# Kernel tuning notes

Measured on AMD Instinct MI355X. Metric: run time of the kernel, lower is better.

## Reference

```python
import jax, jax.numpy as jnp
import numpy as np

EPS = 1e-12  # VERY_SMALL_NUMBER
LN_EPS = 1e-5
N, NFEAT, NHID, A, P, HOPS = 50000, 256, 128, 32, 4, 2


def setup_inputs() -> dict:
    key = jax.random.key(0)
    ks = jax.random.split(key, 16)
    def w(i, shape, scale=0.05):
        return jax.random.normal(ks[i], shape, dtype=jnp.float32) * scale
    return {
        "x": jax.random.normal(ks[0], (N, NFEAT), dtype=jnp.float32),
        # input_mapper: Linear(nfeat,nhid) -> ReLU -> Linear(nhid,nhid)
        "im_w1": w(1, (NFEAT, NHID)), "im_b1": jnp.zeros((NHID,), jnp.float32),
        "im_w2": w(2, (NHID, NHID)),  "im_b2": jnp.zeros((NHID,), jnp.float32),
        # AnchorGraphLearner
        "anchors": w(3, (A, NHID), 1.0),
        "ml_w1": w(4, (P, 2 * NHID, NHID)), "ml_b1": jnp.zeros((P, NHID), jnp.float32),
        "ml_w2": w(5, (P, NHID)),            "ml_b2": jnp.zeros((P,), jnp.float32),
        # AnchorGNNLayer weights (xavier in torch; scaled randn here)
        "enc_w": w(6, (HOPS, NHID, NHID)), "enc_b": jnp.zeros((HOPS, NHID), jnp.float32),
        # LayerNorm
        "ln_g": jnp.ones((NHID,), jnp.float32), "ln_b": jnp.zeros((NHID,), jnp.float32),
        # classifier: Linear -> PReLU(nhid) -> Linear(nhid,2)
        "cls_w1": w(7, (NHID, NHID)), "cls_b1": jnp.zeros((NHID,), jnp.float32),
        "prelu_a": jnp.full((NHID,), 0.25, jnp.float32),
        "cls_w2": w(8, (NHID, 2)),   "cls_b2": jnp.zeros((2,), jnp.float32),
    }


def _forward(x, im_w1, im_b1, im_w2, im_b2, anchors, ml_w1, ml_b1, ml_w2, ml_b2,
             enc_w, enc_b, ln_g, ln_b, cls_w1, cls_b1, prelu_a, cls_w2, cls_b2):
    nhid = im_w2.shape[-1]
    # input_mapper (dropout is identity in eval)
    h = jnp.maximum(x @ im_w1 + im_b1, 0.0) @ im_w2 + im_b2  # [N, nhid]
    x_loc = h

    # --- AnchorGraphLearner: fused form of cat([x_i, a_j]) @ W1 ---
    Wx, Wa = ml_w1[:, :nhid, :], ml_w1[:, nhid:, :]  # each [P, nhid, nhid]
    attn = jnp.zeros((h.shape[0], anchors.shape[0]), h.dtype)
    for p in range(ml_w1.shape[0]):  # small fixed head count
        hx = h @ Wx[p]                               # [N, nhid]
        ha = anchors @ Wa[p]                         # [A, nhid]
        hid = jnp.maximum(hx[:, None, :] + ha[None, :, :] + ml_b1[p], 0.0)  # [N, A, nhid]
        attn = attn + jax.nn.sigmoid(hid @ ml_w2[p] + ml_b2[p])            # [N, A]
    adj = attn / ml_w1.shape[0]  # mean over heads, [N, A]

    # --- AnchorGNNLayer stack (anchor_mp normalized double matmul) ---
    node_norm = adj / jnp.maximum(adj.sum(axis=0, keepdims=True), EPS)     # col-normalized [N, A]
    anchor_norm = adj / jnp.maximum(adj.sum(axis=1, keepdims=True), EPS)   # row-normalized [N, A]
    xc = h
    for i in range(enc_w.shape[0]):
        support = xc @ enc_w[i]                          # [N, nhid]
        agg = node_norm.T @ support                      # [A, nhid]
        xc = jnp.maximum(anchor_norm @ agg + enc_b[i], 0.0)

    # residual + LayerNorm
    z = xc + x_loc
    mu = z.mean(axis=-1, keepdims=True)
    var = ((z - mu) ** 2).mean(axis=-1, keepdims=True)
    z = (z - mu) * jax.lax.rsqrt(var + LN_EPS) * ln_g + ln_b

    def classifier(t):
        t1 = t @ cls_w1 + cls_b1
        t1 = jnp.where(t1 > 0, t1, prelu_a * t1)  # PReLU(nhid)
        return t1 @ cls_w2 + cls_b2

    pred = classifier(z)                 # [N, 2]
    anchor_logits = classifier(anchors)  # [A, 2]
    anchor_vec = anchors[None]           # [1, A, nhid] (matches unsqueeze(0))
    return (pred, z, anchor_vec, anchor_logits)


def reference(x, im_w1, im_b1, im_w2, im_b2, anchors, ml_w1, ml_b1, ml_w2, ml_b2,
              enc_w, enc_b, ln_g, ln_b, cls_w1, cls_b1, prelu_a, cls_w2, cls_b2):
    return _forward(x, im_w1, im_b1, im_w2, im_b2, anchors, ml_w1, ml_b1, ml_w2, ml_b2,
                    enc_w, enc_b, ln_g, ln_b, cls_w1, cls_b1, prelu_a, cls_w2, cls_b2)
```

## Files before the change

kernel.cpp:

```cpp
#include <hip/hip_runtime.h>
#include <math.h>

#define NN 50000
#define FEAT 256
#define HID 128
#define NA 32
#define NP 4
#define TM 64
#define NBLK 782
#define LDA 132
#define EPSS 1e-12f
#define LN_EPS 1e-5f

typedef unsigned short u16;
typedef __attribute__((ext_vector_type(8))) short bf16x8;
typedef __attribute__((ext_vector_type(4))) float f32x4;

#define ADJ_F   0
#define RS_F    1600000
#define CS_F    1650000
#define AGG0_F  1650032
#define AGG1_F  1654128
#define HB_F    1658256
#define FLAG_F  1674640
#define F_END   1674672
#define XC_U   (2 * F_END)
#define SUP_U  (XC_U + NN * HID)
#define PW_U   (SUP_U + NN * HID)
#define PW_TOT 165638
#define WS_NEED_BYTES ((size_t)(PW_U + PW_TOT) * 2ULL)

#define PK_IMW1T  0
#define PK_IMW2T  32768
#define PK_MLW1T  49152
#define PK_ENCWT  114688
#define PK_CLSW1T 147456
#define PK_IMB1   163840
#define PK_IMB2   163968
#define PK_MLW2   164096
#define PK_ENCB   164608
#define PK_LNG    164864
#define PK_LNB    164992
#define PK_CLSB1  165120
#define PK_PRELU  165248
#define PK_CLSW2  165376
#define PK_CLSB2  165632
#define PK_MLB2   165634
#define PK_TOTAL  165638

#define PRED_OFF 0
#define Z_OFF    100000
#define AV_OFF   6500000
#define AL_OFF   6504096
#define OUT_TOT  6504160

__device__ __constant__ int kNel[19] = {
    NN * FEAT, FEAT * HID, HID, HID * HID, HID, NA * HID,
    NP * 2 * HID * HID, NP * HID, NP * HID, NP, 2 * HID * HID, 2 * HID,
    HID, HID, HID * HID, HID, HID, HID * 2, 2};

#define TSEG_TOT 163840
__device__ __constant__ int tLen[9]  = {32768,16384,16384,16384,16384,16384,16384,16384,16384};
__device__ __constant__ int tDst[9]  = {PK_IMW1T,PK_IMW2T,PK_MLW1T,PK_MLW1T+16384,
                                        PK_MLW1T+32768,PK_MLW1T+49152,PK_ENCWT,
                                        PK_ENCWT+16384,PK_CLSW1T};
__device__ __constant__ int tSrcT[9] = {1,3,6,6,6,6,10,10,14};
__device__ __constant__ int tBase[9] = {0,0,0,32768,65536,98304,0,16384,0};
#define VSEG_TOT 1798
__device__ __constant__ int vLen[11] = {128,128,512,256,128,128,128,128,256,2,4};
__device__ __constant__ int vDst[11] = {PK_IMB1,PK_IMB2,PK_MLW2,PK_ENCB,PK_LNG,PK_LNB,
                                        PK_CLSB1,PK_PRELU,PK_CLSW2,PK_CLSB2,PK_MLB2};
__device__ __constant__ int vSrcT[11]= {2,4,8,11,12,13,15,16,17,18,9};

struct P19 { const void* q[19]; };

__device__ __forceinline__ float b2f(u16 u) {
    union { float f; unsigned int i; } v; v.i = ((unsigned int)u) << 16; return v.f;
}
__device__ __forceinline__ u16 f2b(float f) {
    union { float f; unsigned int i; } v; v.f = f;
    unsigned int x = v.i;
    x += 0x7fffu + ((x >> 16) & 1u);
    return (u16)(x >> 16);
}
__device__ __forceinline__ float ldf(const void* p, size_t i, int fl) {
    if (fl == 1) return ((const float*)p)[i];
    if (fl == 0) return b2f(((const u16*)p)[i]);
    return 0.f;
}

__global__ __launch_bounds__(256) void k_detect_all(P19 a, int* __restrict__ flags) {
    __shared__ int sHi[256], sE[256], sO[256];
    const int b = blockIdx.x;
    const u16* p = (const u16*)a.q[b];
    const int M = (kNel[b] < 8192) ? kNel[b] : 8192;
    int cHi = 0, cE = 0, cO = 0;
    for (int j = threadIdx.x; j < M; j += 256) {
        const u16 v = p[j];
        if (j & 1) cO += (v != 0);
        else { cE += (v != 0); cHi += (((v >> 7) & 0xFF) >= 200); }
    }
    sHi[threadIdx.x] = cHi; sE[threadIdx.x] = cE; sO[threadIdx.x] = cO;
    __syncthreads();
    for (int s = 128; s > 0; s >>= 1) {
        if (threadIdx.x < (unsigned)s) {
            sHi[threadIdx.x] += sHi[threadIdx.x + s];
            sE[threadIdx.x]  += sE[threadIdx.x + s];
            sO[threadIdx.x]  += sO[threadIdx.x + s];
        }
        __syncthreads();
    }
    if (threadIdx.x == 0) {
        int f;
        if (sE[0] == 0 && sO[0] == 0) f = 2;
        else if (sHi[0] >= 4 || sE[0] == 0) f = 1;
        else f = 0;
        flags[b] = f;
    }
}

__global__ __launch_bounds__(256) void k_convT(P19 a, const int* __restrict__ flags,
                                               u16* __restrict__ pw) {
    int idx = blockIdx.x * 256 + threadIdx.x;
    if (idx >= TSEG_TOT) return;
    int off = idx, s = 0;
    while (off >= tLen[s]) { off -= tLen[s]; ++s; }
    int n, k;
    if (s == 0) { n = off >> 8; k = off & 255; }
    else        { n = off >> 7; k = off & 127; }
    const int si = tSrcT[s];
    pw[tDst[s] + off] = f2b(ldf(a.q[si], (size_t)tBase[s] + (size_t)k * 128 + n,
                                flags[si]));
}

__global__ __launch_bounds__(256) void k_convV(P19 a, const int* __restrict__ flags,
                                               u16* __restrict__ pw) {
    for (int idx = threadIdx.x; idx < VSEG_TOT; idx += 256) {
        int off = idx, s = 0;
        while (off >= vLen[s]) { off -= vLen[s]; ++s; }
        const int si = vSrcT[s];
        pw[vDst[s] + off] = f2b(ldf(a.q[si], off, flags[si]));
    }
}

__device__ __forceinline__ void mfma_64x128(const u16* As, const u16* Bt,
                                            f32x4 acc[8], int lane, int rowBase) {
    const int lr = lane & 15, lq = lane >> 4;
#pragma unroll
    for (int kc = 0; kc < 4; ++kc) {
        bf16x8 a = *(const bf16x8*)(As + (rowBase + lr) * 136 + kc * 32 + lq * 8);
#pragma unroll
        for (int t = 0; t < 8; ++t) {
            bf16x8 b = *(const bf16x8*)(Bt + (t * 16 + lr) * 136 + kc * 32 + lq * 8);
            acc[t] = __builtin_amdgcn_mfma_f32_16x16x32_bf16(a, b, acc[t], 0, 0, 0);
        }
    }
}

__global__ __launch_bounds__(256) void k_gemm2(const void* __restrict__ A,
                                               const u16* __restrict__ pw,
                                               float* __restrict__ outh,
                                               const int* __restrict__ flags) {
    __shared__ __align__(16) u16 As[64 * 136];
    __shared__ __align__(16) u16 Bt[128 * 136];
    const int fA = flags[0];
    const int tid = threadIdx.x;
    const int row0 = blockIdx.x * TM;
    const int lane = tid & 63, wv = tid >> 6, rowBase = wv * 16;
    const int lr = lane & 15, lq = lane >> 4;
    f32x4 acc[8];
    const f32x4 z4 = {0.f, 0.f, 0.f, 0.f};
#pragma unroll
    for (int t = 0; t < 8; ++t) acc[t] = z4;

    for (int kc = 0; kc < 2; ++kc) {
        for (int i = tid; i < 64 * 32; i += 256) {
            const int m = i >> 5, k4 = (i & 31) << 2;
            const int g = row0 + m;
            ushort4 o; o.x = 0; o.y = 0; o.z = 0; o.w = 0;
            if (g < NN) {
                const size_t idx = (size_t)g * FEAT + kc * 128 + k4;
                if (fA == 1) {
                    float4 v = *(const float4*)((const float*)A + idx);
                    o.x = f2b(v.x); o.y = f2b(v.y); o.z = f2b(v.z); o.w = f2b(v.w);
                } else {
                    o = *(const ushort4*)((const u16*)A + idx);
                }
            }
            *(ushort4*)&As[m * 136 + k4] = o;
        }
        for (int i = tid; i < 128 * 32; i += 256) {
            const int n = i >> 5, k4 = (i & 31) << 2;
            *(ushort4*)&Bt[n * 136 + k4] =
                *(const ushort4*)(pw + PK_IMW1T + (size_t)n * FEAT + kc * 128 + k4);
        }
        __syncthreads();
        mfma_64x128(As, Bt, acc, lane, rowBase);
        __syncthreads();
    }
#pragma unroll
    for (int t = 0; t < 8; ++t) {
        const int col = t * 16 + lr;
        const float bv = b2f(pw[PK_IMB1 + col]);
#pragma unroll
        for (int r = 0; r < 4; ++r)
            As[(rowBase + lq * 4 + r) * 136 + col] = f2b(fmaxf(acc[t][r] + bv, 0.f));
    }
    for (int i = tid; i < 128 * 32; i += 256) {
        const int n = i >> 5, k4 = (i & 31) << 2;
        *(ushort4*)&Bt[n * 136 + k4] =
            *(const ushort4*)(pw + PK_IMW2T + (size_t)n * HID + k4);
    }
    __syncthreads();
    f32x4 acc2[8];
#pragma unroll
    for (int t = 0; t < 8; ++t) acc2[t] = z4;
    mfma_64x128(As, Bt, acc2, lane, rowBase);
#pragma unroll
    for (int t = 0; t < 8; ++t) {
        const int col = t * 16 + lr;
        const float bv = b2f(pw[PK_IMB2 + col]);
#pragma unroll
        for (int r = 0; r < 4; ++r) {
            const int g = row0 + rowBase + lq * 4 + r;
            if (g < NN) outh[(size_t)g * HID + col] = acc2[t][r] + bv;
        }
    }
}

__global__ __launch_bounds__(128) void k_pre(const void* __restrict__ anchors,
                                             const void* __restrict__ ml_w1,
                                             const void* __restrict__ ml_b1,
                                             float* __restrict__ hb,
                                             const int* __restrict__ flags) {
    __shared__ float sa[HID];
    const int fAn = flags[5], fW1 = flags[6], fB1 = flags[7];
    const int p = blockIdx.x >> 5, a = blockIdx.x & 31, k = threadIdx.x;
    sa[k] = ldf(anchors, a * HID + k, fAn);
    __syncthreads();
    float acc = ldf(ml_b1, p * HID + k, fB1);
    const size_t wbase = ((size_t)p * 2 * HID + HID) * HID + k;
#pragma unroll 4
    for (int j = 0; j < HID; ++j)
        acc += sa[j] * ldf(ml_w1, wbase + (size_t)j * HID, fW1);
    hb[p * (NA * HID) + k * NA + a] = acc;
}

__global__ __launch_bounds__(128) void k_wc(const float* __restrict__ hb,
                                            const u16* __restrict__ pw,
                                            float* __restrict__ wc) {
    __shared__ float red[128];
    const int p = blockIdx.x, tid = threadIdx.x;
    const int a = tid & 31, q = tid >> 5;
    float s = 0.f;
    for (int k = q * 32; k < q * 32 + 32; ++k)
        s += b2f(pw[PK_MLW2 + p * HID + k]) * hb[(size_t)p * (NA * HID) + k * NA + a];
    red[tid] = 0.5f * s;
    __syncthreads();
    if (tid < 32)
        wc[p * NA + tid] = red[tid] + red[tid + 32] + red[tid + 64] + red[tid + 96];
}

__global__ __launch_bounds__(256) void k_anchor(const void* __restrict__ anchors,
                                                const void* __restrict__ cls_w1,
                                                const void* __restrict__ cls_b1,
                                                const void* __restrict__ prelu_a,
                                                const void* __restrict__ cls_w2,
                                                const void* __restrict__ cls_b2,
                                                float* __restrict__ out,
                                                const int* __restrict__ flags) {
    __shared__ float sa[2][HID];
    __shared__ float st1[2][HID];
    const int fAn = flags[5], fW1 = flags[14], fB1 = flags[15];
    const int fPa = flags[16], fW2 = flags[17], fB2 = flags[18];
    const int tid = threadIdx.x;
    const int a0 = blockIdx.x * 2;
    const int half = tid >> 7, k = tid & 127;
    sa[half][k] = ldf(anchors, (a0 + half) * HID + k, fAn);
    __syncthreads();
    float acc = ldf(cls_b1, k, fB1);
#pragma unroll 4
    for (int j = 0; j < HID; ++j) acc += sa[half][j] * ldf(cls_w1, j * HID + k, fW1);
    const float pa = ldf(prelu_a, k, fPa);
    st1[half][k] = acc > 0.f ? acc : pa * acc;
    __syncthreads();
    if (tid < 4) {
        const int aa = tid >> 1, c = tid & 1;
        float s = ldf(cls_b2, c, fB2);
        for (int j = 0; j < HID; ++j) s += st1[aa][j] * ldf(cls_w2, j * 2 + c, fW2);
        out[AL_OFF + (a0 + aa) * 2 + c] = s;
    }
    if (blockIdx.x == 0) {
        for (int i = tid; i < NA * HID; i += 256)
            out[AV_OFF + i] = ldf(anchors, i, fAn);
    }
}

__global__ __launch_bounds__(256) void k_fattn(const float* __restrict__ h,
                                               const u16* __restrict__ pw,
                                               const float* __restrict__ hb,
                                               const float* __restrict__ wc,
                                               float* __restrict__ adj,
                                               float* __restrict__ rowsum,
                                               float* __restrict__ csPart,
                                               float* __restrict__ part) {
    __shared__ __align__(16) u16 Bt[128 * 136];
    __shared__ float hws[HID];
    __shared__ float wcs[NA];
    __shared__ float swr[4][NA];
    float* hbf = (float*)&Bt[64 * 136];
    const int tid = threadIdx.x;
    const int row0 = blockIdx.x * TM;
    const int lane = tid & 63, wv = tid >> 6, rowBase = wv * 16;
    const int lr = lane & 15, lq = lane >> 4;
    const int g = tid & 3, myrow = tid >> 2;
    const int a0 = g * 8;

    bf16x8 afr[4];
    {
        const int gr = row0 + rowBase + lr;
#pragma unroll
        for (int kc = 0; kc < 4; ++kc) {
            bf16x8 t;
            if (gr < NN) {
                const float* src = h + (size_t)gr * HID + kc * 32 + lq * 8;
                float4 v0 = *(const float4*)src;
                float4 v1 = *(const float4*)(src + 4);
                t[0] = (short)f2b(v0.x); t[1] = (short)f2b(v0.y);
                t[2] = (short)f2b(v0.z); t[3] = (short)f2b(v0.w);
                t[4] = (short)f2b(v1.x); t[5] = (short)f2b(v1.y);
                t[6] = (short)f2b(v1.z); t[7] = (short)f2b(v1.w);
            } else {
#pragma unroll
                for (int j = 0; j < 8; ++j) t[j] = 0;
            }
            afr[kc] = t;
        }
    }

    float adjacc[8];
#pragma unroll
    for (int j = 0; j < 8; ++j) adjacc[j] = 0.f;

    for (int p = 0; p < NP; ++p) {
        __syncthreads();
        for (int i = tid; i < 128 * 32; i += 256) {
            const int n = i >> 5, k4 = (i & 31) << 2;
            *(ushort4*)&Bt[n * 136 + k4] =
                *(const ushort4*)(pw + PK_MLW1T + p * 16384 + n * 128 + k4);
        }
        if (tid < HID) hws[tid] = 0.5f * b2f(pw[PK_MLW2 + p * HID + tid]);
        if (tid < NA) wcs[tid] = wc[p * NA + tid];
        __syncthreads();

        f32x4 acc[8];
        const f32x4 z4 = {0.f, 0.f, 0.f, 0.f};
#pragma unroll
        for (int t = 0; t < 8; ++t) acc[t] = z4;
#pragma unroll
        for (int kc = 0; kc < 4; ++kc)
#pragma unroll
            for (int t = 0; t < 8; ++t) {
                bf16x8 b = *(const bf16x8*)(Bt + (t * 16 + lr) * 136 + kc * 32 + lq * 8);
                acc[t] = __builtin_amdgcn_mfma_f32_16x16x32_bf16(afr[kc], b, acc[t], 0, 0, 0);
            }
        __syncthreads();
#pragma unroll
        for (int t = 0; t < 8; ++t)
#pragma unroll
            for (int r = 0; r < 4; ++r)
                Bt[(rowBase + lq * 4 + r) * 136 + t * 16 + lr] = f2b(acc[t][r]);
        {
            const float4* hbp4 = (const float4*)(hb + (size_t)p * (NA * HID));
#pragma unroll
            for (int j = 0; j < 4; ++j)
                ((float4*)hbf)[tid + j * 256] = hbp4[tid + j * 256];
        }
        __syncthreads();

        const float b2v = b2f(pw[PK_MLB2 + p]);
        float sabs[8], wh = 0.f;
#pragma unroll
        for (int j = 0; j < 8; ++j) sabs[j] = 0.f;

#pragma unroll 4
        for (int kp = 0; kp < 64; ++kp) {
            const unsigned hx2 = *(const unsigned*)&Bt[myrow * 136 + kp * 2];
            union { unsigned u; float f; } u0, u1;
            u0.u = hx2 << 16;
            u1.u = hx2 & 0xffff0000u;
            const float f0 = u0.f, f1 = u1.f;
            const float2 hw2 = *(const float2*)&hws[kp * 2];
            wh = fmaf(hw2.x, f0, wh);
            wh = fmaf(hw2.y, f1, wh);
            const float4 c00 = *(const float4*)&hbf[(kp * 2) * NA + a0];
            const float4 c01 = *(const float4*)&hbf[(kp * 2) * NA + a0 + 4];
            const float4 c10 = *(const float4*)&hbf[(kp * 2 + 1) * NA + a0];
            const float4 c11 = *(const float4*)&hbf[(kp * 2 + 1) * NA + a0 + 4];
            sabs[0] = fmaf(hw2.x, fabsf(f0 + c00.x), sabs[0]);
            sabs[1] = fmaf(hw2.x, fabsf(f0 + c00.y), sabs[1]);
            sabs[2] = fmaf(hw2.x, fabsf(f0 + c00.z), sabs[2]);
            sabs[3] = fmaf(hw2.x, fabsf(f0 + c00.w), sabs[3]);
            sabs[4] = fmaf(hw2.x, fabsf(f0 + c01.x), sabs[4]);
            sabs[5] = fmaf(hw2.x, fabsf(f0 + c01.y), sabs[5]);
            sabs[6] = fmaf(hw2.x, fabsf(f0 + c01.z), sabs[6]);
            sabs[7] = fmaf(hw2.x, fabsf(f0 + c01.w), sabs[7]);
            sabs[0] = fmaf(hw2.y, fabsf(f1 + c10.x), sabs[0]);
            sabs[1] = fmaf(hw2.y, fabsf(f1 + c10.y), sabs[1]);
            sabs[2] = fmaf(hw2.y, fabsf(f1 + c10.z), sabs[2]);
            sabs[3] = fmaf(hw2.y, fabsf(f1 + c10.w), sabs[3]);
            sabs[4] = fmaf(hw2.y, fabsf(f1 + c11.x), sabs[4]);
            sabs[5] = fmaf(hw2.y, fabsf(f1 + c11.y), sabs[5]);
            sabs[6] = fmaf(hw2.y, fabsf(f1 + c11.z), sabs[6]);
            sabs[7] = fmaf(hw2.y, fabsf(f1 + c11.w), sabs[7]);
        }
#pragma unroll
        for (int j = 0; j < 8; ++j) {
            const float s = wh + wcs[a0 + j] + b2v + sabs[j];
            adjacc[j] += 0.25f / (1.f + __expf(-s));
        }
    }

    const int grow = row0 + myrow;
    if (grow >= NN) {
#pragma unroll
        for (int j = 0; j < 8; ++j) adjacc[j] = 0.f;
    }
    if (grow < NN) {
        float* dst = adj + (size_t)grow * NA + a0;
        *(float4*)dst = make_float4(adjacc[0], adjacc[1], adjacc[2], adjacc[3]);
        *(float4*)(dst + 4) = make_float4(adjacc[4], adjacc[5], adjacc[6], adjacc[7]);
    }
    float rs = 0.f;
#pragma unroll
    for (int j = 0; j < 8; ++j) rs += adjacc[j];
    rs += __shfl_xor(rs, 1);
    rs += __shfl_xor(rs, 2);
    if (g == 0 && grow < NN) rowsum[grow] = rs;
    __syncthreads();
#pragma unroll
    for (int kc = 0; kc < 4; ++kc)
        *(bf16x8*)&Bt[(rowBase + lr) * 136 + kc * 32 + lq * 8] = afr[kc];
    float* adjTe = (float*)&Bt[64 * 136];
#pragma unroll
    for (int j = 0; j < 8; ++j)
        adjTe[myrow * 33 + a0 + j] = adjacc[j];
#pragma unroll
    for (int st = 4; st <= 32; st <<= 1)
#pragma unroll
        for (int j = 0; j < 8; ++j) adjacc[j] += __shfl_xor(adjacc[j], st);
    if (lane < 4) {
#pragma unroll
        for (int j = 0; j < 8; ++j) swr[wv][lane * 8 + j] = adjacc[j];
    }
    __syncthreads();
    if (tid < NA)
        csPart[tid * NBLK + blockIdx.x] =
            swr[0][tid] + swr[1][tid] + swr[2][tid] + swr[3][tid];
    const int aA = (tid & 15) * 2, kA = (tid >> 4) * 8;
    float acc2[2][8];
#pragma unroll
    for (int ia = 0; ia < 2; ++ia)
#pragma unroll
        for (int j = 0; j < 8; ++j) acc2[ia][j] = 0.f;
#pragma unroll 4
    for (int n = 0; n < TM; ++n) {
        const float a0v = adjTe[n * 33 + aA], a1v = adjTe[n * 33 + aA + 1];
        ushort4 u0 = *(const ushort4*)&Bt[n * 136 + kA];
        ushort4 u1 = *(const ushort4*)&Bt[n * 136 + kA + 4];
        float sv[8] = {b2f(u0.x), b2f(u0.y), b2f(u0.z), b2f(u0.w),
                       b2f(u1.x), b2f(u1.y), b2f(u1.z), b2f(u1.w)};
#pragma unroll
        for (int j = 0; j < 8; ++j) {
            acc2[0][j] += a0v * sv[j];
            acc2[1][j] += a1v * sv[j];
        }
    }
    float* pdst = part + (size_t)blockIdx.x * (NA * HID);
#pragma unroll
    for (int ia = 0; ia < 2; ++ia) {
        *(float4*)&pdst[(aA + ia) * HID + kA] =
            make_float4(acc2[ia][0], acc2[ia][1], acc2[ia][2], acc2[ia][3]);
        *(float4*)&pdst[(aA + ia) * HID + kA + 4] =
            make_float4(acc2[ia][4], acc2[ia][5], acc2[ia][6], acc2[ia][7]);
    }
}

__global__ __launch_bounds__(256) void k_cs_red(const float* __restrict__ csPart,
                                                float* __restrict__ colsum) {
    __shared__ float red[256];
    const int a = blockIdx.x, tid = threadIdx.x;
    float s = 0.f;
    for (int b = tid; b < NBLK; b += 256) s += csPart[a * NBLK + b];
    red[tid] = s;
    __syncthreads();
    for (int st = 128; st > 0; st >>= 1) {
        if (tid < st) red[tid] += red[tid + st];
        __syncthreads();
    }
    if (tid == 0) colsum[a] = red[0];
}

__global__ __launch_bounds__(256) void k_Tred(const float* __restrict__ part,
                                              float* __restrict__ T) {
    __shared__ float red[256];
    const int jj = threadIdx.x & 15, bq = threadIdx.x >> 4;
    const int j = blockIdx.x * 16 + jj;
    float s = 0.f;
#pragma unroll 8
    for (int b = bq; b < NBLK; b += 16) s += part[(size_t)b * (NA * HID) + j];
    red[threadIdx.x] = s;
    __syncthreads();
    if (bq == 0) {
        float t = 0.f;
#pragma unroll
        for (int q = 0; q < 16; ++q) t += red[q * 16 + jj];
        T[j] = t;
    }
}

__global__ __launch_bounds__(128) void k_small(const float* __restrict__ T,
                                               const u16* __restrict__ pw,
                                               const int hop,
                                               float* __restrict__ agg) {
    __shared__ float tr[HID];
    const int a = blockIdx.x, n = threadIdx.x;
    tr[n] = T[a * HID + n];
    __syncthreads();
    const u16* w = pw + PK_ENCWT + hop * HID * HID + n * HID;
    float s = 0.f;
#pragma unroll 4
    for (int j4 = 0; j4 < HID; j4 += 4) {
        ushort4 u = *(const ushort4*)(w + j4);
        s += tr[j4] * b2f(u.x) + tr[j4 + 1] * b2f(u.y) +
             tr[j4 + 2] * b2f(u.z) + tr[j4 + 3] * b2f(u.w);
    }
    agg[a * HID + n] = s;
}

__global__ __launch_bounds__(256) void k_e2a(const float* __restrict__ adj,
                                             const float* __restrict__ rowsum,
                                             const float* __restrict__ colsum,
                                             const float* __restrict__ agg,
                                             const u16* __restrict__ pw,
                                             float* __restrict__ part) {
    __shared__ float aggn[NA][LDA];
    __shared__ float adjT[TM][NA + 1];
    __shared__ __align__(8) u16 xcs[TM * 136];
    __shared__ float csl[NA], rsl[TM];
    const int tid = threadIdx.x;
    const int row0 = blockIdx.x * TM;
    const int n0 = (tid & 31) * 4, m0 = (tid >> 5) * 8;
    const int a0 = (tid & 15) * 2, k0 = (tid >> 4) * 8;

    if (tid < NA) csl[tid] = fmaxf(colsum[tid], EPSS);
    if (tid >= 64 && tid < 128) {
        const int m = tid - 64, g = row0 + m;
        rsl[m] = (g < NN) ? 1.f / fmaxf(rowsum[g], EPSS) : 0.f;
    }
    for (int i = tid; i < TM * NA; i += 256) {
        const int m = i >> 5, a = i & 31, g = row0 + m;
        adjT[m][a] = (g < NN) ? adj[(size_t)g * NA + a] : 0.f;
    }
    __syncthreads();
    for (int i = tid; i < (NA * HID) / 4; i += 256) {
        const int a = i >> 5, k4 = (i & 31) << 2;
        float4 v = *(const float4*)(agg + a * HID + k4);
        const float inv = 1.f / csl[a];
        v.x *= inv; v.y *= inv; v.z *= inv; v.w *= inv;
        *(float4*)&aggn[a][k4] = v;
    }
    float bv[4];
#pragma unroll
    for (int j = 0; j < 4; ++j) bv[j] = b2f(pw[PK_ENCB + n0 + j]);
    __syncthreads();
    float acc[8][4];
#pragma unroll
    for (int i = 0; i < 8; ++i)
#pragma unroll
        for (int j = 0; j < 4; ++j) acc[i][j] = 0.f;
    for (int a = 0; a < NA; ++a) {
        float4 gv = *(const float4*)&aggn[a][n0];
        float gvv[4] = {gv.x, gv.y, gv.z, gv.w};
#pragma unroll
        for (int i = 0; i < 8; ++i) {
            const float av = adjT[m0 + i][a];
#pragma unroll
            for (int j = 0; j < 4; ++j) acc[i][j] += av * gvv[j];
        }
    }
#pragma unroll
    for (int i = 0; i < 8; ++i) {
        const float r = rsl[m0 + i];
        ushort4 o;
        o.x = f2b(fmaxf(r * acc[i][0] + bv[0], 0.f));
        o.y = f2b(fmaxf(r * acc[i][1] + bv[1], 0.f));
        o.z = f2b(fmaxf(r * acc[i][2] + bv[2], 0.f));
        o.w = f2b(fmaxf(r * acc[i][3] + bv[3], 0.f));
        *(ushort4*)&xcs[(m0 + i) * 136 + n0] = o;
    }
    __syncthreads();
    float acc2[2][8];
#pragma unroll
    for (int ia = 0; ia < 2; ++ia)
#pragma unroll
        for (int j = 0; j < 8; ++j) acc2[ia][j] = 0.f;
#pragma unroll 4
    for (int n = 0; n < TM; ++n) {
        const float a0v = adjT[n][a0], a1v = adjT[n][a0 + 1];
        ushort4 u0 = *(const ushort4*)&xcs[n * 136 + k0];
        ushort4 u1 = *(const ushort4*)&xcs[n * 136 + k0 + 4];
        float sv[8] = {b2f(u0.x), b2f(u0.y), b2f(u0.z), b2f(u0.w),
                       b2f(u1.x), b2f(u1.y), b2f(u1.z), b2f(u1.w)};
#pragma unroll
        for (int j = 0; j < 8; ++j) {
            acc2[0][j] += a0v * sv[j];
            acc2[1][j] += a1v * sv[j];
        }
    }
    float* dst = part + (size_t)blockIdx.x * (NA * HID);
#pragma unroll
    for (int ia = 0; ia < 2; ++ia) {
        *(float4*)&dst[(a0 + ia) * HID + k0] =
            make_float4(acc2[ia][0], acc2[ia][1], acc2[ia][2], acc2[ia][3]);
        *(float4*)&dst[(a0 + ia) * HID + k0 + 4] =
            make_float4(acc2[ia][4], acc2[ia][5], acc2[ia][6], acc2[ia][7]);
    }
}

__global__ __launch_bounds__(256) void k_e2f(const float* __restrict__ adj,
                                             const float* __restrict__ rowsum,
                                             const float* __restrict__ colsum,
                                             const float* __restrict__ agg,
                                             const u16* __restrict__ pw,
                                             float* __restrict__ out) {
    __shared__ __align__(16) u16 As[64 * 136];
    __shared__ __align__(16) u16 uniB[128 * 136];
    __shared__ float smu[TM], sinv[TM], sg[HID], sb[HID], w2s[2 * HID];
    __shared__ float csl[NA], rsl[TM];
    float* aggn  = (float*)As;
    float* adjTf = (float*)uniB;
    float* zT    = (float*)uniB;
    const int tid = threadIdx.x;
    const int row0 = blockIdx.x * TM;
    const int lane = tid & 63, wv = tid >> 6, rowBase = wv * 16;
    const int lr = lane & 15, lq = lane >> 4;
    const int n0 = (tid & 31) * 4, m0 = (tid >> 5) * 8;
    const float* h = out + Z_OFF;

    if (tid < NA) csl[tid] = fmaxf(colsum[tid], EPSS);
    if (tid >= 64 && tid < 128) {
        const int m = tid - 64, g = row0 + m;
        rsl[m] = (g < NN) ? 1.f / fmaxf(rowsum[g], EPSS) : 0.f;
    }
    for (int i = tid; i < TM * NA; i += 256) {
        const int m = i >> 5, a = i & 31, g = row0 + m;
        adjTf[m * (NA + 1) + a] = (g < NN) ? adj[(size_t)g * NA + a] : 0.f;
    }
    __syncthreads();
    for (int i = tid; i < (NA * HID) / 4; i += 256) {
        const int a = i >> 5, k4 = (i & 31) << 2;
        float4 v = *(const float4*)(agg + a * HID + k4);
        const float inv = 1.f / csl[a];
        v.x *= inv; v.y *= inv; v.z *= inv; v.w *= inv;
        *(float4*)&aggn[a * LDA + k4] = v;
    }
    __syncthreads();
    float acc[8][4];
#pragma unroll
    for (int i = 0; i < 8; ++i)
#pragma unroll
        for (int j = 0; j < 4; ++j) acc[i][j] = 0.f;
    for (int a = 0; a < NA; ++a) {
        float4 gv = *(const float4*)&aggn[a * LDA + n0];
        float gvv[4] = {gv.x, gv.y, gv.z, gv.w};
#pragma unroll
        for (int i = 0; i < 8; ++i) {
            const float av = adjTf[(m0 + i) * (NA + 1) + a];
#pragma unroll
            for (int j = 0; j < 4; ++j) acc[i][j] += av * gvv[j];
        }
    }
    float bv[4];
#pragma unroll
    for (int j = 0; j < 4; ++j) bv[j] = b2f(pw[PK_ENCB + HID + n0 + j]);
    float xcv[8][4];
#pragma unroll
    for (int i = 0; i < 8; ++i) {
        const float r = rsl[m0 + i];
#pragma unroll
        for (int j = 0; j < 4; ++j)
            xcv[i][j] = fmaxf(r * acc[i][j] + bv[j], 0.f);
    }
    __syncthreads();
#pragma unroll
    for (int i = 0; i < 8; ++i) {
        const int g = row0 + m0 + i;
        float4 hv = make_float4(0.f, 0.f, 0.f, 0.f);
        if (g < NN) hv = *(const float4*)(h + (size_t)g * HID + n0);
        float4 zv = make_float4(xcv[i][0] + hv.x, xcv[i][1] + hv.y,
                                xcv[i][2] + hv.z, xcv[i][3] + hv.w);
        *(float4*)&zT[(m0 + i) * 132 + n0] = zv;
    }
    if (tid < HID) { sg[tid] = b2f(pw[PK_LNG + tid]); sb[tid] = b2f(pw[PK_LNB + tid]); }
    w2s[tid] = b2f(pw[PK_CLSW2 + tid]);
    __syncthreads();
    if (tid < TM) {
        float s = 0.f;
        for (int k = 0; k < HID; ++k) s += zT[tid * 132 + k];
        const float mu = s * (1.f / HID);
        float v = 0.f;
        for (int k = 0; k < HID; ++k) { const float d = zT[tid * 132 + k] - mu; v += d * d; }
        smu[tid] = mu;
        sinv[tid] = rsqrtf(v * (1.f / HID) + LN_EPS);
    }
    __syncthreads();
    for (int i = tid; i < TM * 32; i += 256) {
        const int m = i >> 5, k4 = (i & 31) << 2, g = row0 + m;
        float4 v = *(const float4*)&zT[m * 132 + k4];
        const float mu = smu[m], inv = sinv[m];
        v.x = (v.x - mu) * inv * sg[k4 + 0] + sb[k4 + 0];
        v.y = (v.y - mu) * inv * sg[k4 + 1] + sb[k4 + 1];
        v.z = (v.z - mu) * inv * sg[k4 + 2] + sb[k4 + 2];
        v.w = (v.w - mu) * inv * sg[k4 + 3] + sb[k4 + 3];
        if (g < NN) *(float4*)&out[Z_OFF + (size_t)g * HID + k4] = v;
        ushort4 o; o.x = f2b(v.x); o.y = f2b(v.y); o.z = f2b(v.z); o.w = f2b(v.w);
        *(ushort4*)&As[m * 136 + k4] = o;
    }
    __syncthreads();
    for (int i = tid; i < 128 * 32; i += 256) {
        const int n = i >> 5, k4 = (i & 31) << 2;
        *(ushort4*)&uniB[n * 136 + k4] =
            *(const ushort4*)(pw + PK_CLSW1T + n * 128 + k4);
    }
    __syncthreads();
    f32x4 macc[8];
    const f32x4 z4 = {0.f, 0.f, 0.f, 0.f};
#pragma unroll
    for (int t = 0; t < 8; ++t) macc[t] = z4;
    mfma_64x128(As, uniB, macc, lane, rowBase);
    __syncthreads();
#pragma unroll
    for (int t = 0; t < 8; ++t) {
        const int col = t * 16 + lr;
        const float bc = b2f(pw[PK_CLSB1 + col]);
        const float pa = b2f(pw[PK_PRELU + col]);
#pragma unroll
        for (int r = 0; r < 4; ++r) {
            float v = macc[t][r] + bc;
            v = v > 0.f ? v : pa * v;
            As[(rowBase + lq * 4 + r) * 136 + col] = f2b(v);
        }
    }
    __syncthreads();
    if (tid < 128) {
        const int r = tid >> 1, c = tid & 1, g = row0 + r;
        if (g < NN) {
            float s = b2f(pw[PK_CLSB2 + c]);
            for (int k = 0; k < HID; ++k) s += b2f(As[r * 136 + k]) * w2s[k * 2 + c];
            out[PRED_OFF + (size_t)g * 2 + c] = s;
        }
    }
}

extern "C" void kernel_launch(void* const* d_in, const int* in_sizes, int n_in,
                              void* d_out, int out_size, void* d_ws, size_t ws_size,
                              hipStream_t stream) {
    const bool ok = (n_in >= 19) && (out_size == OUT_TOT) &&
                    (ws_size >= WS_NEED_BYTES) &&
                    (in_sizes[0] == NN * FEAT) && (in_sizes[6] == NP * 2 * HID * HID) &&
                    (in_sizes[10] == 2 * HID * HID) && (in_sizes[17] == HID * 2);
    if (!ok) {
        hipMemsetAsync(d_out, 0, (size_t)OUT_TOT * 4, stream);
        return;
    }

    float* ws    = (float*)d_ws;
    u16*   wsu   = (u16*)d_ws;
    float* out   = (float*)d_out;
    int*   flags = (int*)(ws + FLAG_F);
    float* hbuf  = out + Z_OFF;
    u16*   pw    = wsu + PW_U;
    float* xcf   = (float*)(wsu + XC_U);
    float* csPart = xcf;
    float* partb = xcf + 32768;
    float* Tbuf  = ws + HB_F;
    float* wcv   = ws + AGG1_F;

    P19 pa;
    for (int i = 0; i < 19; ++i) pa.q[i] = d_in[i];
    k_detect_all<<<19, 256, 0, stream>>>(pa, flags);
    k_convT<<<(TSEG_TOT + 255) / 256, 256, 0, stream>>>(pa, flags, pw);
    k_convV<<<1, 256, 0, stream>>>(pa, flags, pw);

    k_pre<<<NP * NA, 128, 0, stream>>>(d_in[5], d_in[6], d_in[7], ws + HB_F, flags);
    k_wc<<<NP, 128, 0, stream>>>(ws + HB_F, pw, wcv);
    k_anchor<<<NA / 2, 256, 0, stream>>>(d_in[5], d_in[14], d_in[15], d_in[16],
                                         d_in[17], d_in[18], out, flags);

    k_gemm2<<<NBLK, 256, 0, stream>>>(d_in[0], pw, hbuf, flags);

    k_fattn<<<NBLK, 256, 0, stream>>>(hbuf, pw, ws + HB_F, wcv, ws + ADJ_F,
                                      ws + RS_F, csPart, partb);
    k_cs_red<<<NA, 256, 0, stream>>>(csPart, ws + CS_F);

    k_Tred<<<256, 256, 0, stream>>>(partb, Tbuf);
    k_small<<<NA, 128, 0, stream>>>(Tbuf, pw, 0, ws + AGG0_F);
    k_e2a<<<NBLK, 256, 0, stream>>>(ws + ADJ_F, ws + RS_F, ws + CS_F, ws + AGG0_F,
                                    pw, partb);
    k_Tred<<<256, 256, 0, stream>>>(partb, Tbuf);
    k_small<<<NA, 128, 0, stream>>>(Tbuf, pw, 1, ws + AGG1_F);
    k_e2f<<<NBLK, 256, 0, stream>>>(ws + ADJ_F, ws + RS_F, ws + CS_F, ws + AGG1_F,
                                    pw, out);
}
```

Before: 431.8 us.

## Merge small setup and reduction kernels to cut launch count

Folds the vector-conversion kernel into the weight-transpose kernel as an extra block. The transpose now goes through a shared-memory 32x32 tile so both reads and writes are coalesced. The wc reduction moves into k_pre through a block reduction, and the colsum reduction is merged into the first T-reduction launch as extra blocks. The goal is to remove three kernel launches and the uncoalesced transpose writes, at the cost of slightly more complex per-block dispatch.

```diff
diff --git a/kernel.cpp b/kernel.cpp
--- a/kernel.cpp
+++ b/kernel.cpp
@@ -59,8 +59,6 @@
     NP * 2 * HID * HID, NP * HID, NP * HID, NP, 2 * HID * HID, 2 * HID,
     HID, HID, HID * HID, HID, HID, HID * 2, 2};
 
-#define TSEG_TOT 163840
-__device__ __constant__ int tLen[9]  = {32768,16384,16384,16384,16384,16384,16384,16384,16384};
 __device__ __constant__ int tDst[9]  = {PK_IMW1T,PK_IMW2T,PK_MLW1T,PK_MLW1T+16384,
                                         PK_MLW1T+32768,PK_MLW1T+49152,PK_ENCWT,
                                         PK_ENCWT+16384,PK_CLSW1T};
@@ -121,25 +119,35 @@
 
 __global__ __launch_bounds__(256) void k_convT(P19 a, const int* __restrict__ flags,
                                                u16* __restrict__ pw) {
-    int idx = blockIdx.x * 256 + threadIdx.x;
-    if (idx >= TSEG_TOT) return;
-    int off = idx, s = 0;
-    while (off >= tLen[s]) { off -= tLen[s]; ++s; }
-    int n, k;
-    if (s == 0) { n = off >> 8; k = off & 255; }
-    else        { n = off >> 7; k = off & 127; }
-    const int si = tSrcT[s];
-    pw[tDst[s] + off] = f2b(ldf(a.q[si], (size_t)tBase[s] + (size_t)k * 128 + n,
-                                flags[si]));
-}
-
-__global__ __launch_bounds__(256) void k_convV(P19 a, const int* __restrict__ flags,
-                                               u16* __restrict__ pw) {
-    for (int idx = threadIdx.x; idx < VSEG_TOT; idx += 256) {
-        int off = idx, s = 0;
-        while (off >= vLen[s]) { off -= vLen[s]; ++s; }
-        const int si = vSrcT[s];
-        pw[vDst[s] + off] = f2b(ldf(a.q[si], off, flags[si]));
+    const int b = blockIdx.x;
+    if (b == 160) {
+        for (int idx = threadIdx.x; idx < VSEG_TOT; idx += 256) {
+            int off = idx, s = 0;
+            while (off >= vLen[s]) { off -= vLen[s]; ++s; }
+            const int si = vSrcT[s];
+            pw[vDst[s] + off] = f2b(ldf(a.q[si], off, flags[si]));
+        }
+        return;
+    }
+    __shared__ float tle[32][33];
+    int s, t;
+    if (b < 32) { s = 0; t = b; }
+    else        { s = 1 + (b - 32) / 16; t = (b - 32) % 16; }
+    const int K = (s == 0) ? 256 : 128;
+    const int tn = (t & 3) * 32, tk = (t >> 2) * 32;
+    const int si = tSrcT[s], fl = flags[si];
+    const int c0 = threadIdx.x & 31, q0 = threadIdx.x >> 5;
+#pragma unroll
+    for (int i = 0; i < 4; ++i) {
+        const int kk = q0 + i * 8;
+        tle[kk][c0] = ldf(a.q[si],
+                          (size_t)tBase[s] + (size_t)(tk + kk) * 128 + tn + c0, fl);
+    }
+    __syncthreads();
+#pragma unroll
+    for (int i = 0; i < 4; ++i) {
+        const int nn = q0 + i * 8;
+        pw[tDst[s] + (size_t)(tn + nn) * K + tk + c0] = f2b(tle[c0][nn]);
     }
 }
 
@@ -231,10 +239,13 @@
 __global__ __launch_bounds__(128) void k_pre(const void* __restrict__ anchors,
                                              const void* __restrict__ ml_w1,
                                              const void* __restrict__ ml_b1,
+                                             const void* __restrict__ ml_w2,
                                              float* __restrict__ hb,
+                                             float* __restrict__ wc,
                                              const int* __restrict__ flags) {
     __shared__ float sa[HID];
-    const int fAn = flags[5], fW1 = flags[6], fB1 = flags[7];
+    __shared__ float red[128];
+    const int fAn = flags[5], fW1 = flags[6], fB1 = flags[7], fW2 = flags[8];
     const int p = blockIdx.x >> 5, a = blockIdx.x & 31, k = threadIdx.x;
     sa[k] = ldf(anchors, a * HID + k, fAn);
     __syncthreads();
@@ -244,21 +255,13 @@
     for (int j = 0; j < HID; ++j)
         acc += sa[j] * ldf(ml_w1, wbase + (size_t)j * HID, fW1);
     hb[p * (NA * HID) + k * NA + a] = acc;
-}
-
-__global__ __launch_bounds__(128) void k_wc(const float* __restrict__ hb,
-                                            const u16* __restrict__ pw,
-                                            float* __restrict__ wc) {
-    __shared__ float red[128];
-    const int p = blockIdx.x, tid = threadIdx.x;
-    const int a = tid & 31, q = tid >> 5;
-    float s = 0.f;
-    for (int k = q * 32; k < q * 32 + 32; ++k)
-        s += b2f(pw[PK_MLW2 + p * HID + k]) * hb[(size_t)p * (NA * HID) + k * NA + a];
-    red[tid] = 0.5f * s;
-    __syncthreads();
-    if (tid < 32)
-        wc[p * NA + tid] = red[tid] + red[tid + 32] + red[tid + 64] + red[tid + 96];
+    red[k] = 0.5f * ldf(ml_w2, p * HID + k, fW2) * acc;
+    __syncthreads();
+    for (int st = 64; st > 0; st >>= 1) {
+        if (k < st) red[k] += red[k + st];
+        __syncthreads();
+    }
+    if (k == 0) wc[p * NA + a] = red[0];
 }
 
 __global__ __launch_bounds__(256) void k_anchor(const void* __restrict__ anchors,
@@ -486,30 +489,32 @@
     }
 }
 
-__global__ __launch_bounds__(256) void k_cs_red(const float* __restrict__ csPart,
-                                                float* __restrict__ colsum) {
+template<int WCS>
+__global__ __launch_bounds__(256) void k_Tred(const float* __restrict__ part,
+                                              float* __restrict__ T,
+                                              const float* __restrict__ csPart,
+                                              float* __restrict__ colsum) {
     __shared__ float red[256];
-    const int a = blockIdx.x, tid = threadIdx.x;
-    float s = 0.f;
-    for (int b = tid; b < NBLK; b += 256) s += csPart[a * NBLK + b];
-    red[tid] = s;
-    __syncthreads();
-    for (int st = 128; st > 0; st >>= 1) {
-        if (tid < st) red[tid] += red[tid + st];
+    const int tid = threadIdx.x;
+    if (WCS && blockIdx.x >= 256) {
+        const int a = blockIdx.x - 256;
+        float s = 0.f;
+        for (int b = tid; b < NBLK; b += 256) s += csPart[a * NBLK + b];
+        red[tid] = s;
         __syncthreads();
-    }
-    if (tid == 0) colsum[a] = red[0];
-}
-
-__global__ __launch_bounds__(256) void k_Tred(const float* __restrict__ part,
-                                              float* __restrict__ T) {
-    __shared__ float red[256];
-    const int jj = threadIdx.x & 15, bq = threadIdx.x >> 4;
+        for (int st = 128; st > 0; st >>= 1) {
+            if (tid < st) red[tid] += red[tid + st];
+            __syncthreads();
+        }
+        if (tid == 0) colsum[a] = red[0];
+        return;
+    }
+    const int jj = tid & 15, bq = tid >> 4;
     const int j = blockIdx.x * 16 + jj;
     float s = 0.f;
 #pragma unroll 8
     for (int b = bq; b < NBLK; b += 16) s += part[(size_t)b * (NA * HID) + j];
-    red[threadIdx.x] = s;
+    red[tid] = s;
     __syncthreads();
     if (bq == 0) {
         float t = 0.f;
@@ -790,11 +795,10 @@
     P19 pa;
     for (int i = 0; i < 19; ++i) pa.q[i] = d_in[i];
     k_detect_all<<<19, 256, 0, stream>>>(pa, flags);
-    k_convT<<<(TSEG_TOT + 255) / 256, 256, 0, stream>>>(pa, flags, pw);
-    k_convV<<<1, 256, 0, stream>>>(pa, flags, pw);
-
-    k_pre<<<NP * NA, 128, 0, stream>>>(d_in[5], d_in[6], d_in[7], ws + HB_F, flags);
-    k_wc<<<NP, 128, 0, stream>>>(ws + HB_F, pw, wcv);
+    k_convT<<<161, 256, 0, stream>>>(pa, flags, pw);
+
+    k_pre<<<NP * NA, 128, 0, stream>>>(d_in[5], d_in[6], d_in[7], d_in[8],
+                                       ws + HB_F, wcv, flags);
     k_anchor<<<NA / 2, 256, 0, stream>>>(d_in[5], d_in[14], d_in[15], d_in[16],
                                          d_in[17], d_in[18], out, flags);
 
@@ -802,13 +806,12 @@
 
     k_fattn<<<NBLK, 256, 0, stream>>>(hbuf, pw, ws + HB_F, wcv, ws + ADJ_F,
                                       ws + RS_F, csPart, partb);
-    k_cs_red<<<NA, 256, 0, stream>>>(csPart, ws + CS_F);
-
-    k_Tred<<<256, 256, 0, stream>>>(partb, Tbuf);
+
+    k_Tred<1><<<288, 256, 0, stream>>>(partb, Tbuf, csPart, ws + CS_F);
     k_small<<<NA, 128, 0, stream>>>(Tbuf, pw, 0, ws + AGG0_F);
     k_e2a<<<NBLK, 256, 0, stream>>>(ws + ADJ_F, ws + RS_F, ws + CS_F, ws + AGG0_F,
                                     pw, partb);
-    k_Tred<<<256, 256, 0, stream>>>(partb, Tbuf);
+    k_Tred<0><<<256, 256, 0, stream>>>(partb, Tbuf, csPart, ws + CS_F);
     k_small<<<NA, 128, 0, stream>>>(Tbuf, pw, 1, ws + AGG1_F);
     k_e2f<<<NBLK, 256, 0, stream>>>(ws + ADJ_F, ws + RS_F, ws + CS_F, ws + AGG1_F,
                                     pw, out);
```

New measurement: 417.8 us. -3.2%, faster.
